# Kernel tuning notes

Measured on AMD Instinct MI355X. Metric: run time of the kernel, lower is better.

Reference implementation:

```python
import jax, jax.numpy as jnp
import numpy as np

N = 100000      # nodes
E = 1600000     # edges (before self-loops)
F_IN = 128
H1, C1 = 8, 8   # layer 1: 8 heads x 8 channels
H2, C2 = 1, 64  # layer 2: 1 head x 64 channels
NEG_SLOPE = 0.2


def setup_inputs() -> dict:
    key = jax.random.key(0)
    ks = jax.random.split(key, 10)
    x = jax.random.normal(ks[0], (N, F_IN), jnp.float32)
    edge_index = jax.random.randint(ks[1], (2, E), 0, N, dtype=jnp.int32)
    s1 = 1.0 / np.sqrt(F_IN)
    s2 = 1.0 / np.sqrt(H1 * C1)
    return {
        "x": x,
        "edge_index": edge_index,
        "W1": jax.random.normal(ks[2], (F_IN, H1 * C1), jnp.float32) * s1,
        "a_src1": jax.random.normal(ks[3], (H1, C1), jnp.float32) * s1,
        "a_dst1": jax.random.normal(ks[4], (H1, C1), jnp.float32) * s1,
        "b1": jnp.zeros((H1 * C1,), jnp.float32),
        "W2": jax.random.normal(ks[5], (H1 * C1, H2 * C2), jnp.float32) * s2,
        "a_src2": jax.random.normal(ks[6], (H2, C2), jnp.float32) * s2,
        "a_dst2": jax.random.normal(ks[7], (H2, C2), jnp.float32) * s2,
        "b2": jnp.zeros((C2,), jnp.float32),
    }


def gat_conv(x, W, a_src, a_dst, b, src, dst, heads, out_ch, concat):
    """PyG-style GATConv (eval mode, self-loops already in src/dst)."""
    n = x.shape[0]
    h = (x @ W).reshape(n, heads, out_ch)            # [N, H, C]
    alpha_s = jnp.sum(h * a_src, axis=-1)            # [N, H]
    alpha_d = jnp.sum(h * a_dst, axis=-1)            # [N, H]
    e = alpha_s[src] + alpha_d[dst]                  # [E, H]
    e = jnp.where(e > 0, e, NEG_SLOPE * e)           # leaky relu
    # segment softmax grouped by destination node
    m = jax.ops.segment_max(e, dst, num_segments=n)  # [N, H]
    m = jnp.where(jnp.isfinite(m), m, 0.0)
    p = jnp.exp(e - m[dst])                          # [E, H]
    denom = jax.ops.segment_sum(p, dst, num_segments=n)
    alpha = p / (denom[dst] + 1e-16)                 # [E, H]
    # weighted scatter-add aggregation
    out = jax.ops.segment_sum(h[src] * alpha[:, :, None], dst, num_segments=n)
    out = out.reshape(n, heads * out_ch) if concat else out.mean(axis=1)
    return out + b


def reference(x, edge_index, W1, a_src1, a_dst1, b1, W2, a_src2, a_dst2, b2):
    n = x.shape[0]
    loops = jnp.arange(n, dtype=edge_index.dtype)    # PyG adds self-loops
    src = jnp.concatenate([edge_index[0], loops])
    dst = jnp.concatenate([edge_index[1], loops])
    h = gat_conv(x, W1, a_src1, a_dst1, b1, src, dst, H1, C1, True)
    h = jax.nn.elu(h)
    h = gat_conv(h, W2, a_src2, a_dst2, b2, src, dst, H2, C2, False)
    return jax.nn.log_softmax(h, axis=1)
```

## Files before the change

kernel.cpp:

```cpp
#include <hip/hip_runtime.h>
#include <math.h>

#define NEG_SLOPE 0.2f
#define CHUNK 4096
#define NPART 64
#define SLICECAP 128
#define CAP 48

typedef __attribute__((ext_vector_type(8))) short bf16x8;
typedef __attribute__((ext_vector_type(4))) float f32x4;

__device__ __forceinline__ unsigned short f2bf(float f) {
    unsigned int u = __float_as_uint(f);
    unsigned int r = (u + 0x7FFFu + ((u >> 16) & 1u)) >> 16;
    return (unsigned short)r;
}
__device__ __forceinline__ float bfl(unsigned int u) { return __uint_as_float(u << 16); }
__device__ __forceinline__ float bfh(unsigned int u) { return __uint_as_float(u & 0xffff0000u); }

__global__ void bucket_slice(const int* __restrict__ ei, int E, int nchunks, int PR,
                             int2* __restrict__ qds, int* __restrict__ scnt) {
    __shared__ int lcnt[8][NPART];
    __shared__ int lbase[8][NPART];
    int tid = threadIdx.x, wave = tid >> 6;
    int chunk = blockIdx.x;
    int base = chunk * CHUNK;
    for (int i = tid; i < 8 * NPART; i += 512) ((int*)lcnt)[i] = 0;
    __syncthreads();
    int d[8], s[8], b[8], pos[8];
    #pragma unroll
    for (int k = 0; k < 8; ++k) {
        int t = base + k * 512 + tid;
        bool v = t < E;
        d[k] = v ? ei[E + t] : 0;
        s[k] = v ? ei[t] : 0;
        b[k] = v ? (d[k] / PR) : -1;
    }
    #pragma unroll
    for (int k = 0; k < 8; ++k)
        pos[k] = (b[k] >= 0) ? atomicAdd(&lcnt[wave][b[k]], 1) : 0;
    __syncthreads();
    if (tid < NPART) {
        int run = 0;
        #pragma unroll
        for (int w = 0; w < 8; ++w) { lbase[w][tid] = run; run += lcnt[w][tid]; }
        scnt[tid * nchunks + chunk] = run;
    }
    __syncthreads();
    #pragma unroll
    for (int k = 0; k < 8; ++k) {
        if (b[k] >= 0) {
            int p = lbase[wave][b[k]] + pos[k];
            if (p < SLICECAP)
                qds[(size_t)(b[k] * nchunks + chunk) * SLICECAP + p] = make_int2(d[k], s[k]);
        }
    }
}

__global__ void scatter_lds(const int2* __restrict__ qds, const int* __restrict__ scnt,
                            int nchunks, int PR, int N,
                            int* __restrict__ cnt, int* __restrict__ col) {
    extern __shared__ int lc[];
    int b = blockIdx.x;
    int lo = b * PR;
    int tid = threadIdx.x, lane = tid & 63, wave = tid >> 6;
    int nwaves = blockDim.x >> 6;
    for (int i = tid; i < PR; i += blockDim.x) lc[i] = 0;
    __syncthreads();
    for (int sl = wave; sl < nchunks; sl += nwaves) {
        int n = min(scnt[b * nchunks + sl], SLICECAP);
        const int2* q = qds + (size_t)(b * nchunks + sl) * SLICECAP;
        for (int i = lane; i < n; i += 64) {
            int2 e = q[i];
            int p = atomicAdd(&lc[e.x - lo], 1);
            if (p < CAP - 1)
                col[e.x * CAP + p] = e.y;
        }
    }
    __syncthreads();
    for (int i = tid; i < PR; i += blockDim.x) {
        int d = lo + i;
        if (d < N) {
            int p = min(lc[i], CAP - 1);
            col[d * CAP + p] = d;
            cnt[d] = p + 1;
        }
    }
}

template<int K, typename AT>
__global__ __launch_bounds__(256) void gemm_mfma(const AT* __restrict__ A,
                                                 const float* __restrict__ W,
                                                 unsigned short* __restrict__ Hb, int N) {
    constexpr int LD = K + 8;
    __shared__ __align__(16) unsigned short Wt[64 * LD];
    __shared__ __align__(16) unsigned short Xl[64 * LD];
    const int tid = threadIdx.x;
    const int lane = tid & 63, wave = tid >> 6;
    const int l16 = lane & 15, q = lane >> 4;
    for (int i = tid; i < K * 64; i += 256) {
        int k = i >> 6, c = i & 63;
        Wt[c * LD + k] = f2bf(W[i]);
    }
    __syncthreads();
    for (int rb = blockIdx.x; rb * 64 < N; rb += gridDim.x) {
        int r0 = rb * 64;
        if (sizeof(AT) == 4) {
            const float* Af = (const float*)A;
            for (int i = tid; i < 64 * (K / 4); i += 256) {
                int row = i / (K / 4), kq = i % (K / 4);
                int rg = min(r0 + row, N - 1);
                float4 a = *(const float4*)&Af[(size_t)rg * K + kq * 4];
                unsigned short* p = &Xl[row * LD + kq * 4];
                p[0] = f2bf(a.x); p[1] = f2bf(a.y); p[2] = f2bf(a.z); p[3] = f2bf(a.w);
            }
        } else {
            const unsigned short* Ab = (const unsigned short*)A;
            for (int i = tid; i < 64 * (K / 8); i += 256) {
                int row = i / (K / 8), k8 = i % (K / 8);
                int rg = min(r0 + row, N - 1);
                uint4 a = *(const uint4*)&Ab[(size_t)rg * K + k8 * 8];
                *(uint4*)&Xl[row * LD + k8 * 8] = a;
            }
        }
        __syncthreads();
        f32x4 acc[4] = {{0.f,0.f,0.f,0.f},{0.f,0.f,0.f,0.f},{0.f,0.f,0.f,0.f},{0.f,0.f,0.f,0.f}};
        #pragma unroll
        for (int kk = 0; kk < K / 32; ++kk) {
            bf16x8 af = *(bf16x8*)&Xl[(wave * 16 + l16) * LD + kk * 32 + q * 8];
            #pragma unroll
            for (int c = 0; c < 4; ++c) {
                bf16x8 bfr = *(bf16x8*)&Wt[(c * 16 + l16) * LD + kk * 32 + q * 8];
                acc[c] = __builtin_amdgcn_mfma_f32_16x16x32_bf16(af, bfr, acc[c], 0, 0, 0);
            }
        }
        #pragma unroll
        for (int c = 0; c < 4; ++c)
            #pragma unroll
            for (int r = 0; r < 4; ++r)
                Xl[(wave * 16 + q * 4 + r) * LD + c * 16 + l16] = f2bf(acc[c][r]);
        int lrow = wave * 16 + (lane >> 2);
        int lcol = (lane & 3) * 16;
        int node = r0 + lrow;
        uint4 o0 = *(uint4*)&Xl[lrow * LD + lcol];
        uint4 o1 = *(uint4*)&Xl[lrow * LD + lcol + 8];
        if (node < N) {
            *(uint4*)&Hb[(size_t)node * 64 + lcol] = o0;
            *(uint4*)&Hb[(size_t)node * 64 + lcol + 8] = o1;
        }
        __syncthreads();
    }
}

template<int H>
__global__ void alpha_k(const uint4* __restrict__ Hb, const float* __restrict__ a_src,
                        const float* __restrict__ a_dst, float* __restrict__ AS,
                        float* __restrict__ AD, int N) {
    int lane = threadIdx.x & 63;
    int wid = (blockIdx.x * blockDim.x + threadIdx.x) >> 6;
    int nw = (gridDim.x * blockDim.x) >> 6;
    int slot = lane >> 3, l8 = lane & 7;
    float4 as0 = *(const float4*)&a_src[l8 * 8], as1 = *(const float4*)&a_src[l8 * 8 + 4];
    float4 ad0 = *(const float4*)&a_dst[l8 * 8], ad1 = *(const float4*)&a_dst[l8 * 8 + 4];
    for (int n0 = wid * 8; n0 < N; n0 += nw * 8) {
        int n = n0 + slot;
        bool ok = n < N;
        int nc = ok ? n : (N - 1);
        uint4 hv = Hb[(size_t)nc * 8 + l8];
        float s = bfl(hv.x)*as0.x + bfh(hv.x)*as0.y + bfl(hv.y)*as0.z + bfh(hv.y)*as0.w
                + bfl(hv.z)*as1.x + bfh(hv.z)*as1.y + bfl(hv.w)*as1.z + bfh(hv.w)*as1.w;
        float d = bfl(hv.x)*ad0.x + bfh(hv.x)*ad0.y + bfl(hv.y)*ad0.z + bfh(hv.y)*ad0.w
                + bfl(hv.z)*ad1.x + bfh(hv.z)*ad1.y + bfl(hv.w)*ad1.z + bfh(hv.w)*ad1.w;
        if (H == 8) {
            if (ok) { AS[(size_t)nc * 8 + l8] = s; AD[(size_t)nc * 8 + l8] = d; }
        } else {
            #pragma unroll
            for (int off = 1; off <= 4; off <<= 1) {
                s += __shfl_xor(s, off, 64);
                d += __shfl_xor(d, off, 64);
            }
            if (l8 == 0 && ok) { AS[nc] = s; AD[nc] = d; }
        }
    }
}

template<int H, bool FINAL>
__global__ __launch_bounds__(256, 4) void aggregate(
                          const int* __restrict__ cnt, const int* __restrict__ col,
                          const float* __restrict__ AS, const float* __restrict__ AD,
                          const uint4* __restrict__ Hb, const float* __restrict__ bias,
                          void* __restrict__ OUT, int N) {
    int lane = threadIdx.x & 63;
    int wid = (blockIdx.x * blockDim.x + threadIdx.x) >> 6;
    int nw = (gridDim.x * blockDim.x) >> 6;
    int slot = lane >> 3, l8 = lane & 7;
    const int h = (H == 8) ? l8 : 0;
    float4 b4a = *(const float4*)&bias[l8 * 8];
    float4 b4b = *(const float4*)&bias[l8 * 8 + 4];
    for (int nb0 = wid * 8; nb0 < N; nb0 += nw * 8) {
        int n = nb0 + slot;
        bool nok = n < N;
        int nc = nok ? n : (N - 1);
        int beg = nc * CAP;
        int deg = cnt[nc];
        float ad = AD[(size_t)nc * H + h];
        int maxd = deg;
        #pragma unroll
        for (int off = 8; off <= 32; off <<= 1)
            maxd = max(maxd, __shfl_xor(maxd, off, 64));
        float den = 0.0f;
        float acc[8] = {0.f, 0.f, 0.f, 0.f, 0.f, 0.f, 0.f, 0.f};
        int myc = (l8 < deg) ? col[beg + l8] : -1;
        for (int j0 = 0; j0 < maxd; j0 += 8) {
            int mnext = (j0 + 8 + l8 < deg) ? col[beg + j0 + 8 + l8] : -1;
            int sarr[8];
            #pragma unroll
            for (int jj = 0; jj < 8; ++jj)
                sarr[jj] = __shfl(myc, slot * 8 + jj, 64);
            float ev[8];
            uint4 hvv[8];
            #pragma unroll
            for (int jj = 0; jj < 8; ++jj) {
                if (sarr[jj] >= 0) {
                    ev[jj]  = AS[(size_t)sarr[jj] * H + h];
                    hvv[jj] = Hb[(size_t)sarr[jj] * 8 + l8];
                }
            }
            #pragma unroll
            for (int jj = 0; jj < 8; ++jj) {
                if (sarr[jj] >= 0) {
                    float e = ev[jj] + ad;
                    e = e > 0.0f ? e : NEG_SLOPE * e;
                    float p = __expf(e);
                    den += p;
                    uint4 hv = hvv[jj];
                    acc[0] = fmaf(p, bfl(hv.x), acc[0]);
                    acc[1] = fmaf(p, bfh(hv.x), acc[1]);
                    acc[2] = fmaf(p, bfl(hv.y), acc[2]);
                    acc[3] = fmaf(p, bfh(hv.y), acc[3]);
                    acc[4] = fmaf(p, bfl(hv.z), acc[4]);
                    acc[5] = fmaf(p, bfh(hv.z), acc[5]);
                    acc[6] = fmaf(p, bfl(hv.w), acc[6]);
                    acc[7] = fmaf(p, bfh(hv.w), acc[7]);
                }
            }
            myc = mnext;
        }
        float inv = 1.0f / (den + 1e-16f);
        float v[8];
        v[0] = acc[0] * inv + b4a.x; v[1] = acc[1] * inv + b4a.y;
        v[2] = acc[2] * inv + b4a.z; v[3] = acc[3] * inv + b4a.w;
        v[4] = acc[4] * inv + b4b.x; v[5] = acc[5] * inv + b4b.y;
        v[6] = acc[6] * inv + b4b.z; v[7] = acc[7] * inv + b4b.w;
        if (!FINAL) {
            #pragma unroll
            for (int i = 0; i < 8; ++i) v[i] = v[i] > 0.0f ? v[i] : __expf(v[i]) - 1.0f;
            if (nok) {
                union { unsigned short u[8]; uint4 q; } pk;
                #pragma unroll
                for (int i = 0; i < 8; ++i) pk.u[i] = f2bf(v[i]);
                ((uint4*)OUT)[(size_t)n * 8 + l8] = pk.q;
            }
        } else {
            float m = v[0];
            #pragma unroll
            for (int i = 1; i < 8; ++i) m = fmaxf(m, v[i]);
            #pragma unroll
            for (int off = 1; off <= 4; off <<= 1) m = fmaxf(m, __shfl_xor(m, off, 64));
            float ss = 0.0f;
            #pragma unroll
            for (int i = 0; i < 8; ++i) ss += __expf(v[i] - m);
            #pragma unroll
            for (int off = 1; off <= 4; off <<= 1) ss += __shfl_xor(ss, off, 64);
            float lse = m + __logf(ss);
            if (nok) {
                float* Of = (float*)OUT;
                float4 o0 = {v[0] - lse, v[1] - lse, v[2] - lse, v[3] - lse};
                float4 o1 = {v[4] - lse, v[5] - lse, v[6] - lse, v[7] - lse};
                *(float4*)&Of[(size_t)n * 64 + l8 * 8] = o0;
                *(float4*)&Of[(size_t)n * 64 + l8 * 8 + 4] = o1;
            }
        }
    }
}

extern "C" void kernel_launch(void* const* d_in, const int* in_sizes, int n_in,
                              void* d_out, int out_size, void* d_ws, size_t ws_size,
                              hipStream_t stream) {
    const float* x    = (const float*)d_in[0];
    const int*   ei   = (const int*)d_in[1];
    const float* W1   = (const float*)d_in[2];
    const float* as1w = (const float*)d_in[3];
    const float* ad1w = (const float*)d_in[4];
    const float* b1   = (const float*)d_in[5];
    const float* W2   = (const float*)d_in[6];
    const float* as2w = (const float*)d_in[7];
    const float* ad2w = (const float*)d_in[8];
    const float* b2   = (const float*)d_in[9];
    const int N = in_sizes[0] / 128;
    const int E = in_sizes[1] / 2;
    const int nchunks = (E + CHUNK - 1) / CHUNK;
    const int PR = (N + NPART - 1) / NPART;

    float* ws = (float*)d_ws;
    size_t off = 0;
    unsigned short* AGG1b = (unsigned short*)(ws + off); off += (size_t)N * 32;
    unsigned short* h1b   = (unsigned short*)(ws + off); off += (size_t)N * 32;
    unsigned short* h2b   = (unsigned short*)(ws + off); off += (size_t)N * 32;
    int2* qds = (int2*)ws;
    float* AS1  = ws + off; off += (size_t)N * 8;
    float* AD1  = ws + off; off += (size_t)N * 8;
    float* AS2  = ws + off; off += N;
    float* AD2  = ws + off; off += N;
    int* cnt    = (int*)(ws + off);
    int* scnt   = cnt + N;
    int* col    = scnt + NPART * nchunks;

    bucket_slice<<<nchunks, 512, 0, stream>>>(ei, E, nchunks, PR, qds, scnt);
    scatter_lds<<<NPART, 1024, PR * sizeof(int), stream>>>(qds, scnt, nchunks,
                                                           PR, N, cnt, col);

    gemm_mfma<128, float><<<1563, 256, 0, stream>>>(x, W1, h1b, N);
    alpha_k<8><<<782, 256, 0, stream>>>((const uint4*)h1b, as1w, ad1w, AS1, AD1, N);
    aggregate<8, false><<<3125, 256, 0, stream>>>(cnt, col, AS1, AD1,
                                                  (const uint4*)h1b, b1, AGG1b, N);
    gemm_mfma<64, unsigned short><<<1563, 256, 0, stream>>>(AGG1b, W2, h2b, N);
    alpha_k<1><<<782, 256, 0, stream>>>((const uint4*)h2b, as2w, ad2w, AS2, AD2, N);
    aggregate<1, true><<<3125, 256, 0, stream>>>(cnt, col, AS2, AD2,
                                                 (const uint4*)h2b, b2, d_out, N);
}
```

Measured before the change: 267.1 us.

## Fuse attention coefficients into GEMM epilogue and double-buffer aggregation gathers

Attention logits are now computed inside the MFMA GEMM epilogue from the bf16 output tile, so the separate alpha kernels and their re-read of H are gone. The aggregation loop is restructured to process 16 neighbours per iteration with two register buffers, issuing the next batch of gathers before computing on the current one. The aggregate grid also shrinks from 3125 to 1024 blocks, which become persistent-style grid-stride blocks. This costs more registers, which may reduce occupancy.

After: 324.9 us. +21.6%, slower.

```diff
diff --git a/kernel.cpp b/kernel.cpp
--- a/kernel.cpp
+++ b/kernel.cpp
@@ -6,6 +6,7 @@
 #define NPART 64
 #define SLICECAP 128
 #define CAP 48
+#define AGG_GRID 1024
 
 typedef __attribute__((ext_vector_type(8))) short bf16x8;
 typedef __attribute__((ext_vector_type(4))) float f32x4;
@@ -88,20 +89,33 @@
     }
 }
 
-template<int K, typename AT>
+template<int K, int H, typename AT>
 __global__ __launch_bounds__(256) void gemm_mfma(const AT* __restrict__ A,
                                                  const float* __restrict__ W,
-                                                 unsigned short* __restrict__ Hb, int N) {
+                                                 unsigned short* __restrict__ Hb,
+                                                 const float* __restrict__ a_src,
+                                                 const float* __restrict__ a_dst,
+                                                 float* __restrict__ AS,
+                                                 float* __restrict__ AD, int N) {
     constexpr int LD = K + 8;
     __shared__ __align__(16) unsigned short Wt[64 * LD];
     __shared__ __align__(16) unsigned short Xl[64 * LD];
     const int tid = threadIdx.x;
     const int lane = tid & 63, wave = tid >> 6;
     const int l16 = lane & 15, q = lane >> 4;
+    const int lcol = (lane & 3) * 16;
     for (int i = tid; i < K * 64; i += 256) {
         int k = i >> 6, c = i & 63;
         Wt[c * LD + k] = f2bf(W[i]);
     }
+    float4 asv0 = *(const float4*)&a_src[lcol];
+    float4 asv1 = *(const float4*)&a_src[lcol + 4];
+    float4 asv2 = *(const float4*)&a_src[lcol + 8];
+    float4 asv3 = *(const float4*)&a_src[lcol + 12];
+    float4 adv0 = *(const float4*)&a_dst[lcol];
+    float4 adv1 = *(const float4*)&a_dst[lcol + 4];
+    float4 adv2 = *(const float4*)&a_dst[lcol + 8];
+    float4 adv3 = *(const float4*)&a_dst[lcol + 12];
     __syncthreads();
     for (int rb = blockIdx.x; rb * 64 < N; rb += gridDim.x) {
         int r0 = rb * 64;
@@ -140,47 +154,33 @@
             for (int r = 0; r < 4; ++r)
                 Xl[(wave * 16 + q * 4 + r) * LD + c * 16 + l16] = f2bf(acc[c][r]);
         int lrow = wave * 16 + (lane >> 2);
-        int lcol = (lane & 3) * 16;
         int node = r0 + lrow;
         uint4 o0 = *(uint4*)&Xl[lrow * LD + lcol];
         uint4 o1 = *(uint4*)&Xl[lrow * LD + lcol + 8];
         if (node < N) {
             *(uint4*)&Hb[(size_t)node * 64 + lcol] = o0;
             *(uint4*)&Hb[(size_t)node * 64 + lcol + 8] = o1;
+            float sl = bfl(o0.x)*asv0.x + bfh(o0.x)*asv0.y + bfl(o0.y)*asv0.z + bfh(o0.y)*asv0.w
+                     + bfl(o0.z)*asv1.x + bfh(o0.z)*asv1.y + bfl(o0.w)*asv1.z + bfh(o0.w)*asv1.w;
+            float sh = bfl(o1.x)*asv2.x + bfh(o1.x)*asv2.y + bfl(o1.y)*asv2.z + bfh(o1.y)*asv2.w
+                     + bfl(o1.z)*asv3.x + bfh(o1.z)*asv3.y + bfl(o1.w)*asv3.z + bfh(o1.w)*asv3.w;
+            float dl = bfl(o0.x)*adv0.x + bfh(o0.x)*adv0.y + bfl(o0.y)*adv0.z + bfh(o0.y)*adv0.w
+                     + bfl(o0.z)*adv1.x + bfh(o0.z)*adv1.y + bfl(o0.w)*adv1.z + bfh(o0.w)*adv1.w;
+            float dh = bfl(o1.x)*adv2.x + bfh(o1.x)*adv2.y + bfl(o1.y)*adv2.z + bfh(o1.y)*adv2.w
+                     + bfl(o1.z)*adv3.x + bfh(o1.z)*adv3.y + bfl(o1.w)*adv3.z + bfh(o1.w)*adv3.w;
+            if (H == 8) {
+                float2 sv = {sl, sh};
+                float2 dv = {dl, dh};
+                *(float2*)&AS[(size_t)node * 8 + (lane & 3) * 2] = sv;
+                *(float2*)&AD[(size_t)node * 8 + (lane & 3) * 2] = dv;
+            } else {
+                float s = sl + sh, d = dl + dh;
+                s += __shfl_xor(s, 1, 64); s += __shfl_xor(s, 2, 64);
+                d += __shfl_xor(d, 1, 64); d += __shfl_xor(d, 2, 64);
+                if ((lane & 3) == 0) { AS[node] = s; AD[node] = d; }
+            }
         }
         __syncthreads();
-    }
-}
-
-template<int H>
-__global__ void alpha_k(const uint4* __restrict__ Hb, const float* __restrict__ a_src,
-                        const float* __restrict__ a_dst, float* __restrict__ AS,
-                        float* __restrict__ AD, int N) {
-    int lane = threadIdx.x & 63;
-    int wid = (blockIdx.x * blockDim.x + threadIdx.x) >> 6;
-    int nw = (gridDim.x * blockDim.x) >> 6;
-    int slot = lane >> 3, l8 = lane & 7;
-    float4 as0 = *(const float4*)&a_src[l8 * 8], as1 = *(const float4*)&a_src[l8 * 8 + 4];
-    float4 ad0 = *(const float4*)&a_dst[l8 * 8], ad1 = *(const float4*)&a_dst[l8 * 8 + 4];
-    for (int n0 = wid * 8; n0 < N; n0 += nw * 8) {
-        int n = n0 + slot;
-        bool ok = n < N;
-        int nc = ok ? n : (N - 1);
-        uint4 hv = Hb[(size_t)nc * 8 + l8];
-        float s = bfl(hv.x)*as0.x + bfh(hv.x)*as0.y + bfl(hv.y)*as0.z + bfh(hv.y)*as0.w
-                + bfl(hv.z)*as1.x + bfh(hv.z)*as1.y + bfl(hv.w)*as1.z + bfh(hv.w)*as1.w;
-        float d = bfl(hv.x)*ad0.x + bfh(hv.x)*ad0.y + bfl(hv.y)*ad0.z + bfh(hv.y)*ad0.w
-                + bfl(hv.z)*ad1.x + bfh(hv.z)*ad1.y + bfl(hv.w)*ad1.z + bfh(hv.w)*ad1.w;
-        if (H == 8) {
-            if (ok) { AS[(size_t)nc * 8 + l8] = s; AD[(size_t)nc * 8 + l8] = d; }
-        } else {
-            #pragma unroll
-            for (int off = 1; off <= 4; off <<= 1) {
-                s += __shfl_xor(s, off, 64);
-                d += __shfl_xor(d, off, 64);
-            }
-            if (l8 == 0 && ok) { AS[nc] = s; AD[nc] = d; }
-        }
     }
 }
 
@@ -210,42 +210,69 @@
             maxd = max(maxd, __shfl_xor(maxd, off, 64));
         float den = 0.0f;
         float acc[8] = {0.f, 0.f, 0.f, 0.f, 0.f, 0.f, 0.f, 0.f};
-        int myc = (l8 < deg) ? col[beg + l8] : -1;
-        for (int j0 = 0; j0 < maxd; j0 += 8) {
-            int mnext = (j0 + 8 + l8 < deg) ? col[beg + j0 + 8 + l8] : -1;
-            int sarr[8];
-            #pragma unroll
-            for (int jj = 0; jj < 8; ++jj)
-                sarr[jj] = __shfl(myc, slot * 8 + jj, 64);
-            float ev[8];
-            uint4 hvv[8];
+
+        int mycA = (l8 < deg) ? col[beg + l8] : -1;
+        int sA[8];
+        #pragma unroll
+        for (int jj = 0; jj < 8; ++jj) sA[jj] = __shfl(mycA, slot * 8 + jj, 64);
+        float evA[8]; uint4 hvA[8];
+        #pragma unroll
+        for (int jj = 0; jj < 8; ++jj) {
+            if (sA[jj] >= 0) {
+                evA[jj] = AS[(size_t)sA[jj] * H + h];
+                hvA[jj] = Hb[(size_t)sA[jj] * 8 + l8];
+            }
+        }
+        int mycB = (8 + l8 < deg) ? col[beg + 8 + l8] : -1;
+
+#define AGG_COMPUTE(S, EV, HV)                                          \
+        _Pragma("unroll")                                               \
+        for (int jj = 0; jj < 8; ++jj) {                                \
+            if (S[jj] >= 0) {                                           \
+                float e = EV[jj] + ad;                                  \
+                e = e > 0.0f ? e : NEG_SLOPE * e;                       \
+                float p = __expf(e);                                    \
+                den += p;                                               \
+                uint4 hv = HV[jj];                                      \
+                acc[0] = fmaf(p, bfl(hv.x), acc[0]);                    \
+                acc[1] = fmaf(p, bfh(hv.x), acc[1]);                    \
+                acc[2] = fmaf(p, bfl(hv.y), acc[2]);                    \
+                acc[3] = fmaf(p, bfh(hv.y), acc[3]);                    \
+                acc[4] = fmaf(p, bfl(hv.z), acc[4]);                    \
+                acc[5] = fmaf(p, bfh(hv.z), acc[5]);                    \
+                acc[6] = fmaf(p, bfl(hv.w), acc[6]);                    \
+                acc[7] = fmaf(p, bfh(hv.w), acc[7]);                    \
+            }                                                           \
+        }
+
+        for (int j0 = 0; j0 < maxd; j0 += 16) {
+            int sB[8];
+            #pragma unroll
+            for (int jj = 0; jj < 8; ++jj) sB[jj] = __shfl(mycB, slot * 8 + jj, 64);
+            float evB[8]; uint4 hvB[8];
             #pragma unroll
             for (int jj = 0; jj < 8; ++jj) {
-                if (sarr[jj] >= 0) {
-                    ev[jj]  = AS[(size_t)sarr[jj] * H + h];
-                    hvv[jj] = Hb[(size_t)sarr[jj] * 8 + l8];
+                if (sB[jj] >= 0) {
+                    evB[jj] = AS[(size_t)sB[jj] * H + h];
+                    hvB[jj] = Hb[(size_t)sB[jj] * 8 + l8];
                 }
             }
+            int mycC = (j0 + 16 + l8 < deg) ? col[beg + j0 + 16 + l8] : -1;
+            AGG_COMPUTE(sA, evA, hvA)
+            #pragma unroll
+            for (int jj = 0; jj < 8; ++jj) sA[jj] = __shfl(mycC, slot * 8 + jj, 64);
             #pragma unroll
             for (int jj = 0; jj < 8; ++jj) {
-                if (sarr[jj] >= 0) {
-                    float e = ev[jj] + ad;
-                    e = e > 0.0f ? e : NEG_SLOPE * e;
-                    float p = __expf(e);
-                    den += p;
-                    uint4 hv = hvv[jj];
-                    acc[0] = fmaf(p, bfl(hv.x), acc[0]);
-                    acc[1] = fmaf(p, bfh(hv.x), acc[1]);
-                    acc[2] = fmaf(p, bfl(hv.y), acc[2]);
-                    acc[3] = fmaf(p, bfh(hv.y), acc[3]);
-                    acc[4] = fmaf(p, bfl(hv.z), acc[4]);
-                    acc[5] = fmaf(p, bfh(hv.z), acc[5]);
-                    acc[6] = fmaf(p, bfl(hv.w), acc[6]);
-                    acc[7] = fmaf(p, bfh(hv.w), acc[7]);
+                if (sA[jj] >= 0) {
+                    evA[jj] = AS[(size_t)sA[jj] * H + h];
+                    hvA[jj] = Hb[(size_t)sA[jj] * 8 + l8];
                 }
             }
-            myc = mnext;
-        }
+            mycB = (j0 + 24 + l8 < deg) ? col[beg + j0 + 24 + l8] : -1;
+            AGG_COMPUTE(sB, evB, hvB)
+        }
+#undef AGG_COMPUTE
+
         float inv = 1.0f / (den + 1e-16f);
         float v[8];
         v[0] = acc[0] * inv + b4a.x; v[1] = acc[1] * inv + b4a.y;
@@ -320,12 +347,12 @@
     scatter_lds<<<NPART, 1024, PR * sizeof(int), stream>>>(qds, scnt, nchunks,
                                                            PR, N, cnt, col);
 
-    gemm_mfma<128, float><<<1563, 256, 0, stream>>>(x, W1, h1b, N);
-    alpha_k<8><<<782, 256, 0, stream>>>((const uint4*)h1b, as1w, ad1w, AS1, AD1, N);
-    aggregate<8, false><<<3125, 256, 0, stream>>>(cnt, col, AS1, AD1,
-                                                  (const uint4*)h1b, b1, AGG1b, N);
-    gemm_mfma<64, unsigned short><<<1563, 256, 0, stream>>>(AGG1b, W2, h2b, N);
-    alpha_k<1><<<782, 256, 0, stream>>>((const uint4*)h2b, as2w, ad2w, AS2, AD2, N);
-    aggregate<1, true><<<3125, 256, 0, stream>>>(cnt, col, AS2, AD2,
-                                                 (const uint4*)h2b, b2, d_out, N);
-}
+    gemm_mfma<128, 8, float><<<1563, 256, 0, stream>>>(x, W1, h1b, as1w, ad1w,
+                                                       AS1, AD1, N);
+    aggregate<8, false><<<AGG_GRID, 256, 0, stream>>>(cnt, col, AS1, AD1,
+                                                      (const uint4*)h1b, b1, AGG1b, N);
+    gemm_mfma<64, 1, unsigned short><<<1563, 256, 0, stream>>>(AGG1b, W2, h2b,
+                                                               as2w, ad2w, AS2, AD2, N);
+    aggregate<1, true><<<AGG_GRID, 256, 0, stream>>>(cnt, col, AS2, AD2,
+                                                     (const uint4*)h2b, b2, d_out, N);
+}
```
